# Optimization experiments

Hardware: AMD Instinct MI355X
Metric: run time of the kernel (lower is better)

Reference implementation:

```python
import jax, jax.numpy as jnp
import numpy as np


def _maxpool2x2(x):
    # x: [N, C, H, W] -> [N, C, H//2, W//2]
    return jax.lax.reduce_window(x, -jnp.inf, jax.lax.max,
                                 (1, 1, 2, 2), (1, 1, 2, 2), 'VALID')


def _head(a, W1, b1, W2, b2, W3, b3):
    # headModel: maxpool -> (adaptive avgpool to 7x7 is identity here) -> flatten -> classifier (eval mode)
    mp = _maxpool2x2(a)                      # [N, 512, 7, 7]
    flat = mp.reshape(mp.shape[0], -1)       # [N, 25088]
    h = jax.nn.relu(flat @ W1.T + b1)        # [N, 4096]
    h = jax.nn.relu(h @ W2.T + b2)           # [N, 4096]
    return h @ W3.T + b3                     # [N, 1000]


def setup_inputs() -> dict:
    key = jax.random.key(0)
    ks = jax.random.split(key, 7)
    C, HW, FC, NC = 512, 14, 4096, 1000
    acts = jax.random.uniform(ks[0], (1, C, HW, HW), dtype=jnp.float32)  # post-ReLU feature map
    s1 = 1.0 / np.sqrt(C * 7 * 7)
    s2 = 1.0 / np.sqrt(FC)
    return {
        'activations': acts,
        'W1': jax.random.normal(ks[1], (FC, C * 7 * 7), dtype=jnp.float32) * s1,
        'b1': jax.random.normal(ks[2], (FC,), dtype=jnp.float32) * 0.01,
        'W2': jax.random.normal(ks[3], (FC, FC), dtype=jnp.float32) * s2,
        'b2': jax.random.normal(ks[4], (FC,), dtype=jnp.float32) * 0.01,
        'W3': jax.random.normal(ks[5], (NC, FC), dtype=jnp.float32) * s2,
        'b3': jax.random.normal(ks[6], (NC,), dtype=jnp.float32) * 0.01,
        'ht': 224,
        'wt': 224,
    }


def reference(activations, W1, b1, W2, b2, W3, b3, ht, wt):
    C = activations.shape[1]
    logits = _head(activations, W1, b1, W2, b2, W3, b3)   # [1, 1000]
    img_class = jnp.argmax(logits[0])
    base = logits[0, img_class]

    # Batch all C channel ablations: abl[i] = activations with channel i zeroed.
    mask = (1.0 - jnp.eye(C, dtype=activations.dtype))[:, :, None, None]  # [C, C, 1, 1]
    abl = activations * mask                                              # [C, C, 14, 14]
    logits_new = _head(abl, W1, b1, W2, b2, W3, b3)                        # [C, 1000]
    alpha = (base - jnp.take(logits_new, img_class, axis=1)) / base        # [C]

    # fused = relu(sum_i alpha_i * bilinear_resize(act_i)); resize is linear,
    # so weight in activation space and do one resize (same math as the loop).
    weighted = jnp.einsum('c,chw->hw', alpha, activations[0])              # [14, 14]
    sal = jax.image.resize(weighted[None, None], (1, 1, ht, wt),
                           method='bilinear')[0, 0]                        # [ht, wt]
    fused = jax.nn.relu(sal)
    mn, mx = fused.min(), fused.max()
    denom = jnp.where(mx != mn, mx - mn, 1.0)
    fused = jnp.where(mx != mn, (fused - mn) / denom, fused)
    return fused, img_class
```

## Files before the change

kernel.cpp:

```cpp
#include <hip/hip_runtime.h>
#include <math.h>

#define CCH 512
#define F1 25088
#define FC 4096
#define NCLS 1000
#define OW 224
#define KSPLIT 4
#define KSLICE 1024
#define PSTRIDE (CCH*FC)

#define WS_DT 0
#define WS_MP (WS_DT + FC*CCH)
#define WS_QS (WS_MP + F1)
#define WS_H1PRE (WS_QS + FC*4)
#define WS_H1 (WS_H1PRE + FC)
#define WS_H2 (WS_H1 + FC)
#define WS_LOGITS (WS_H2 + FC)
#define WS_CLSBASE (WS_LOGITS + NCLS)
#define WS_ALPHA (WS_CLSBASE + 2)
#define WS_MINMAX (WS_ALPHA + CCH)
#define WS_WEIGHTED (WS_MINMAX + 2)
#define WS_LOGPART (WS_WEIGHTED + 196)
#define WS_A (WS_LOGPART + 64*CCH)
#define WS_PART (WS_A + CCH*FC/2)
#define WS_END (WS_PART + KSPLIT*CCH*FC)
#define WS_NEED_BYTES ((size_t)WS_END * 4)

typedef __attribute__((ext_vector_type(8))) short bfrag;
typedef __attribute__((ext_vector_type(4))) float f32x4;

static __device__ __forceinline__ unsigned short f2bf(float x) {
    unsigned u = __float_as_uint(x);
    unsigned r = 0x7FFFu + ((u >> 16) & 1u);
    return (unsigned short)((u + r) >> 16);
}

#define GLD16(g, l) __builtin_amdgcn_global_load_lds( \
    (const __attribute__((address_space(1))) void*)(g), \
    (__attribute__((address_space(3))) void*)(l), 16, 0, 0)

__global__ void k_maxpool(const float* __restrict__ act, float* __restrict__ ws) {
    int t = threadIdx.x;
    if (blockIdx.x == 0) {
        if (t == 0) ((int*)(ws + WS_MINMAX))[0] = 0x7F800000;
        if (t == 1) ((int*)(ws + WS_MINMAX))[1] = 0;
    }
    int idx = blockIdx.x * 256 + t;
    if (idx >= CCH * 49) return;
    int c = idx / 49, r = idx % 49, y = r / 7, x = r % 7;
    const float* a = act + c * 196 + (2 * y) * 14 + 2 * x;
    float m = fmaxf(fmaxf(a[0], a[1]), fmaxf(a[14], a[15]));
    ws[WS_MP + idx] = m;
}

__global__ __launch_bounds__(256) void k_phi3(const float* __restrict__ W1,
                                              const float* __restrict__ mp,
                                              float* __restrict__ Dt,
                                              float* __restrict__ qs) {
    __shared__ float buf[6272];
    __shared__ float red[128];
    int b = blockIdx.x;
    int j = b >> 2, q = b & 3;
    int t = threadIdx.x;
    const float4* src = (const float4*)(W1 + (size_t)j * F1 + q * 6272);
    const float4* msc = (const float4*)(mp + q * 6272);
    for (int n = t; n < 1568; n += 256) {
        float4 w = src[n], m = msc[n];
        float4 p;
        p.x = w.x * m.x; p.y = w.y * m.y; p.z = w.z * m.z; p.w = w.w * m.w;
        *(float4*)&buf[n * 4] = p;
    }
    __syncthreads();
    if (t < 128) {
        const float* bb = buf + t * 49;
        float s = 0.f;
        #pragma unroll
        for (int k = 0; k < 49; ++k) s += bb[k];
        Dt[(size_t)j * CCH + q * 128 + t] = s;
        red[t] = s;
    }
    __syncthreads();
    if (t < 64) {
        float v = red[t] + red[t + 64];
        for (int off = 32; off > 0; off >>= 1) v += __shfl_down(v, off, 64);
        if (t == 0) qs[b] = v;
    }
}

__global__ void k_h1b(const float* __restrict__ qs, const float* __restrict__ b1,
                      float* __restrict__ h1pre, float* __restrict__ h1) {
    int j = blockIdx.x * 256 + threadIdx.x;
    if (j < FC) {
        const float* g = qs + j * 4;
        float v = b1[j] + ((g[0] + g[1]) + (g[2] + g[3]));
        h1pre[j] = v; h1[j] = fmaxf(v, 0.f);
    }
}

template <bool RELU>
__global__ void k_gemv4096(const float* __restrict__ M, const float* __restrict__ v,
                           const float* __restrict__ bias, float* __restrict__ out) {
    int j = blockIdx.x, t = threadIdx.x;
    const float4* row = (const float4*)(M + (size_t)j * FC);
    const float4* vv = (const float4*)v;
    float s = 0.f;
    #pragma unroll
    for (int q = 0; q < 4; ++q) {
        int n = q * 256 + t;
        float4 w = row[n], x = vv[n];
        s += w.x * x.x + w.y * x.y + w.z * x.z + w.w * x.w;
    }
    __shared__ float red[256];
    red[t] = s; __syncthreads();
    if (t < 128) red[t] += red[t + 128]; __syncthreads();
    if (t < 64)  red[t] += red[t + 64];  __syncthreads();
    if (t < 64) {
        float x = red[t];
        for (int off = 32; off > 0; off >>= 1) x += __shfl_down(x, off, 64);
        if (t == 0) { float r = bias[j] + x; out[j] = RELU ? fmaxf(r, 0.f) : r; }
    }
}

__global__ void k_argmax(const float* __restrict__ logits, float* __restrict__ clsbase,
                         float* __restrict__ dout_cls) {
    int t = threadIdx.x;
    float best = -INFINITY; int bi = NCLS;
    for (int n = t; n < NCLS; n += 256) {
        float v = logits[n];
        if (v > best || (v == best && n < bi)) { best = v; bi = n; }
    }
    __shared__ float bv[256]; __shared__ int bidx[256];
    bv[t] = best; bidx[t] = bi; __syncthreads();
    for (int o = 128; o > 0; o >>= 1) {
        if (t < o) {
            float v2 = bv[t + o]; int i2 = bidx[t + o];
            if (v2 > bv[t] || (v2 == bv[t] && i2 < bidx[t])) { bv[t] = v2; bidx[t] = i2; }
        }
        __syncthreads();
    }
    if (t == 0) { clsbase[0] = (float)bidx[0]; clsbase[1] = bv[0]; *dout_cls = (float)bidx[0]; }
}

__global__ __launch_bounds__(256) void k_abuild(const float* __restrict__ Dt,
                                                const float* __restrict__ h1pre,
                                                unsigned short* __restrict__ A) {
    __shared__ unsigned short tile[64][72];
    int kt = blockIdx.x, it = blockIdx.y, t = threadIdx.x;
    int k0 = kt * 64, i0 = it * 64;
    #pragma unroll
    for (int q = 0; q < 16; ++q) {
        int kk = q * 4 + (t >> 6);
        int ii = t & 63;
        float v = fmaxf(h1pre[k0 + kk] - Dt[(size_t)(k0 + kk) * CCH + i0 + ii], 0.f);
        tile[kk][ii] = f2bf(v);
    }
    __syncthreads();
    #pragma unroll
    for (int q = 0; q < 4; ++q) {
        int c = q * 256 + t;
        int ii = c >> 4, kc = c & 15;
        ushort4 v;
        v.x = tile[kc * 4 + 0][ii]; v.y = tile[kc * 4 + 1][ii];
        v.z = tile[kc * 4 + 2][ii]; v.w = tile[kc * 4 + 3][ii];
        *(ushort4*)&A[(size_t)(i0 + ii) * FC + k0 + kc * 4] = v;
    }
}

__global__ __launch_bounds__(512) void k_mfma_all(
    const unsigned short* __restrict__ A, const float* __restrict__ W2,
    float* __restrict__ part) {
    __shared__ char As[65536];
    __shared__ char Bs[8192];
    int nj = blockIdx.x;
    int ks = blockIdx.y;
    int t = threadIdx.x;
    int wid = t >> 6, lane = t & 63, lr = lane & 15, lh = lane >> 4;
    int j0 = nj * 64;

    int wrow = t >> 3, wch = t & 7;
    const float* wsrc = W2 + (size_t)(j0 + wrow) * FC + (size_t)ks * KSLICE + wch * 8;
    char* bdst = Bs + ((size_t)wrow * 8 + (wch ^ (wrow & 7))) * 16;

    f32x4 acc[4][4];
    #pragma unroll
    for (int f = 0; f < 4; ++f)
        #pragma unroll
        for (int n = 0; n < 4; ++n) acc[f][n] = (f32x4){0.f, 0.f, 0.f, 0.f};

    for (int kst = 0; kst < KSLICE; kst += 64) {
        size_t k0 = (size_t)ks * KSLICE + kst;
        __syncthreads();
        #pragma unroll
        for (int r = 0; r < 8; ++r) {
            int c = t + 512 * r;
            int row = c >> 3, ch = c & 7;
            size_t g = (size_t)row * FC + k0 + (size_t)((ch ^ (row & 7)) * 8);
            GLD16(A + g, As + (size_t)c * 16);
        }
        {
            const float4 wa = ((const float4*)(wsrc + kst))[0];
            const float4 wb = ((const float4*)(wsrc + kst))[1];
            union { bfrag v; unsigned short u[8]; } pk;
            pk.u[0] = f2bf(wa.x); pk.u[1] = f2bf(wa.y);
            pk.u[2] = f2bf(wa.z); pk.u[3] = f2bf(wa.w);
            pk.u[4] = f2bf(wb.x); pk.u[5] = f2bf(wb.y);
            pk.u[6] = f2bf(wb.z); pk.u[7] = f2bf(wb.w);
            *(bfrag*)bdst = pk.v;
        }
        __syncthreads();
        #pragma unroll
        for (int kf = 0; kf < 2; ++kf) {
            bfrag bfr[4];
            #pragma unroll
            for (int n = 0; n < 4; ++n) {
                int brow = n * 16 + lr;
                bfr[n] = *(const bfrag*)(Bs + ((size_t)brow * 8 + ((kf * 4 + lh) ^ (brow & 7))) * 16);
            }
            #pragma unroll
            for (int f = 0; f < 4; ++f) {
                int arow = wid * 64 + f * 16 + lr;
                bfrag af = *(const bfrag*)(As + ((size_t)arow * 8 + ((kf * 4 + lh) ^ (arow & 7))) * 16);
                #pragma unroll
                for (int n = 0; n < 4; ++n)
                    acc[f][n] = __builtin_amdgcn_mfma_f32_16x16x32_bf16(af, bfr[n], acc[f][n], 0, 0, 0);
            }
        }
    }
    float* base = part + (size_t)ks * PSTRIDE;
    #pragma unroll
    for (int f = 0; f < 4; ++f) {
        #pragma unroll
        for (int n = 0; n < 4; ++n) {
            #pragma unroll
            for (int r = 0; r < 4; ++r) {
                int row = wid * 64 + f * 16 + lh * 4 + r;
                base[(size_t)row * FC + j0 + n * 16 + lr] = acc[f][n][r];
            }
        }
    }
}

__global__ __launch_bounds__(256) void k_alpha(
    const float* __restrict__ part, const float* __restrict__ b2,
    const float* __restrict__ W3, const float* __restrict__ b3,
    const float* __restrict__ clsbase, float* __restrict__ alpha) {
    int i = blockIdx.x, t = threadIdx.x;
    int cls = (int)clsbase[0]; float base = clsbase[1];
    const float* w3r = W3 + (size_t)cls * FC;
    const float* p0 = part + (size_t)i * FC;
    float s = 0.f;
    for (int j = t; j < FC; j += 256) {
        float v = ((p0[j] + p0[j + PSTRIDE]) + (p0[j + 2 * PSTRIDE] + p0[j + 3 * PSTRIDE]))
                  + b2[j];
        s += fmaxf(v, 0.f) * w3r[j];
    }
    __shared__ float red[256];
    red[t] = s; __syncthreads();
    if (t < 128) red[t] += red[t + 128]; __syncthreads();
    if (t < 64)  red[t] += red[t + 64];  __syncthreads();
    if (t < 64) {
        float x = red[t];
        for (int off = 32; off > 0; off >>= 1) x += __shfl_down(x, off, 64);
        if (t == 0) {
            float logit = x + b3[cls];
            alpha[i] = (base - logit) / base;
        }
    }
}

__global__ void k_weighted2(const float* __restrict__ alpha, const float* __restrict__ act,
                            float* __restrict__ weighted) {
    __shared__ float sA[CCH];
    int t = threadIdx.x;
    for (int i = t; i < CCH; i += 256) sA[i] = alpha[i];
    __syncthreads();
    for (int p = t; p < 196; p += 256) {
        float s = 0.f;
        for (int i = 0; i < CCH; ++i) s = fmaf(sA[i], act[i * 196 + p], s);
        weighted[p] = s;
    }
}

__global__ __launch_bounds__(256) void k_gemm_abl(
    const float* __restrict__ Dt, const float* __restrict__ h1pre,
    const float* __restrict__ W2, const float* __restrict__ b2,
    const float* __restrict__ W3, const float* __restrict__ clsbase,
    float* __restrict__ logit_part) {
    int mi = blockIdx.x, nj = blockIdx.y, t = threadIdx.x;
    int tx = t & 15, ty = t >> 4;
    int i0 = mi * 64, j0 = nj * 64;
    __shared__ float As2[16][64];
    __shared__ float Bs2[16][65];
    float acc[4][4] = {};
    for (int k0 = 0; k0 < FC; k0 += 16) {
        #pragma unroll
        for (int r = 0; r < 4; ++r) {
            int e = t + 256 * r; int kk = e >> 6, ii = e & 63;
            As2[kk][ii] = fmaxf(h1pre[k0 + kk] - Dt[(size_t)(k0 + kk) * CCH + i0 + ii], 0.f);
        }
        {
            int jj = t >> 2, kks = (t & 3) * 4;
            const float4 wv = *(const float4*)(W2 + (size_t)(j0 + jj) * FC + k0 + kks);
            Bs2[kks + 0][jj] = wv.x; Bs2[kks + 1][jj] = wv.y;
            Bs2[kks + 2][jj] = wv.z; Bs2[kks + 3][jj] = wv.w;
        }
        __syncthreads();
        #pragma unroll
        for (int kk = 0; kk < 16; ++kk) {
            float4 a4 = *(const float4*)&As2[kk][tx * 4];
            float av[4] = {a4.x, a4.y, a4.z, a4.w};
            float bv[4] = {Bs2[kk][ty * 4 + 0], Bs2[kk][ty * 4 + 1],
                           Bs2[kk][ty * 4 + 2], Bs2[kk][ty * 4 + 3]};
            #pragma unroll
            for (int a = 0; a < 4; ++a)
                #pragma unroll
                for (int b = 0; b < 4; ++b)
                    acc[a][b] = fmaf(av[a], bv[b], acc[a][b]);
        }
        __syncthreads();
    }
    int cls = (int)clsbase[0];
    const float* w3r = W3 + (size_t)cls * FC;
    float prt[4] = {0.f, 0.f, 0.f, 0.f};
    #pragma unroll
    for (int b = 0; b < 4; ++b) {
        int j2 = j0 + ty * 4 + b;
        float bb = b2[j2], w3 = w3r[j2];
        #pragma unroll
        for (int a = 0; a < 4; ++a) prt[a] = fmaf(fmaxf(acc[a][b] + bb, 0.f), w3, prt[a]);
    }
    __shared__ float red2[16][68];
    #pragma unroll
    for (int a = 0; a < 4; ++a) red2[ty][tx * 4 + a] = prt[a];
    __syncthreads();
    if (t < 64) {
        float s = 0.f;
        #pragma unroll
        for (int q = 0; q < 16; ++q) s += red2[q][t];
        logit_part[nj * CCH + i0 + t] = s;
    }
}

__global__ void k_alpha_fb(const float* __restrict__ logit_part, const float* __restrict__ b3,
                           const float* __restrict__ clsbase, float* __restrict__ alpha) {
    int t = blockIdx.x * 256 + threadIdx.x;
    if (t >= CCH) return;
    int cls = (int)clsbase[0]; float base = clsbase[1];
    float s = 0.f;
    for (int q = 0; q < 64; ++q) s += logit_part[q * CCH + t];
    alpha[t] = (base - (s + b3[cls])) / base;
}

__global__ void k_resize(const float* __restrict__ weighted, float* __restrict__ out,
                         int* __restrict__ minmax) {
    __shared__ float sW[196];
    int t = threadIdx.x;
    if (t < 196) sW[t] = weighted[t];
    __syncthreads();
    int pix = blockIdx.x * 256 + t;
    int y = pix / OW, x = pix % OW;
    float uy = (y + 0.5f) * 0.0625f - 0.5f;
    float ux = (x + 0.5f) * 0.0625f - 0.5f;
    float y0f = floorf(uy), x0f = floorf(ux);
    float fy = uy - y0f, fx = ux - x0f;
    int y0 = (int)y0f, x0 = (int)x0f;
    int y0c = min(max(y0, 0), 13), y1c = min(max(y0 + 1, 0), 13);
    int x0c = min(max(x0, 0), 13), x1c = min(max(x0 + 1, 0), 13);
    float v00 = sW[y0c * 14 + x0c], v01 = sW[y0c * 14 + x1c];
    float v10 = sW[y1c * 14 + x0c], v11 = sW[y1c * 14 + x1c];
    float v0 = v00 + (v01 - v00) * fx;
    float v1 = v10 + (v11 - v10) * fx;
    float v = v0 + (v1 - v0) * fy;
    float f = fmaxf(v, 0.f);
    out[pix] = f;
    __shared__ float rmn[256], rmx[256];
    rmn[t] = f; rmx[t] = f; __syncthreads();
    for (int o = 128; o > 0; o >>= 1) {
        if (t < o) { rmn[t] = fminf(rmn[t], rmn[t + o]); rmx[t] = fmaxf(rmx[t], rmx[t + o]); }
        __syncthreads();
    }
    if (t == 0) {
        atomicMin(&minmax[0], __float_as_int(rmn[0]));
        atomicMax(&minmax[1], __float_as_int(rmx[0]));
    }
}

__global__ void k_norm(float* __restrict__ out, const int* __restrict__ minmax) {
    float mn = __int_as_float(minmax[0]);
    float mx = __int_as_float(minmax[1]);
    int pix = blockIdx.x * 256 + threadIdx.x;
    if (mx != mn) out[pix] = (out[pix] - mn) / (mx - mn);
}

extern "C" void kernel_launch(void* const* d_in, const int* in_sizes, int n_in,
                              void* d_out, int out_size, void* d_ws, size_t ws_size,
                              hipStream_t stream) {
    const float* act = (const float*)d_in[0];
    const float* W1  = (const float*)d_in[1];
    const float* b1  = (const float*)d_in[2];
    const float* W2  = (const float*)d_in[3];
    const float* b2  = (const float*)d_in[4];
    const float* W3  = (const float*)d_in[5];
    const float* b3  = (const float*)d_in[6];
    float* out = (float*)d_out;
    float* ws = (float*)d_ws;
    const bool fast = (ws_size >= WS_NEED_BYTES);

    k_maxpool<<<98, 256, 0, stream>>>(act, ws);
    k_phi3<<<16384, 256, 0, stream>>>(W1, ws + WS_MP, ws + WS_DT, ws + WS_QS);
    k_h1b<<<16, 256, 0, stream>>>(ws + WS_QS, b1, ws + WS_H1PRE, ws + WS_H1);
    k_gemv4096<true><<<4096, 256, 0, stream>>>(W2, ws + WS_H1, b2, ws + WS_H2);
    k_gemv4096<false><<<1000, 256, 0, stream>>>(W3, ws + WS_H2, b3, ws + WS_LOGITS);
    k_argmax<<<1, 256, 0, stream>>>(ws + WS_LOGITS, ws + WS_CLSBASE, out + 50176);
    if (fast) {
        k_abuild<<<dim3(64, 8), 256, 0, stream>>>(ws + WS_DT, ws + WS_H1PRE,
                                                  (unsigned short*)(ws + WS_A));
        k_mfma_all<<<dim3(64, KSPLIT), 512, 0, stream>>>(
            (const unsigned short*)(ws + WS_A), W2, ws + WS_PART);
        k_alpha<<<CCH, 256, 0, stream>>>(ws + WS_PART, b2, W3, b3,
                                         ws + WS_CLSBASE, ws + WS_ALPHA);
    } else {
        k_gemm_abl<<<dim3(8, 64), 256, 0, stream>>>(ws + WS_DT, ws + WS_H1PRE, W2, b2, W3,
                                                    ws + WS_CLSBASE, ws + WS_LOGPART);
        k_alpha_fb<<<2, 256, 0, stream>>>(ws + WS_LOGPART, b3, ws + WS_CLSBASE,
                                          ws + WS_ALPHA);
    }
    k_weighted2<<<1, 256, 0, stream>>>(ws + WS_ALPHA, act, ws + WS_WEIGHTED);
    k_resize<<<196, 256, 0, stream>>>(ws + WS_WEIGHTED, out, (int*)(ws + WS_MINMAX));
    k_norm<<<196, 256, 0, stream>>>(out, (const int*)(ws + WS_MINMAX));
}
```

Measured before the change: 219.1 us.

## Fuse unablated layer-2 GEMV into batched MFMA kernel and split W1 reduction finer

The baseline layer-2 GEMV (h1·W2) now runs inside the batched ablation MFMA kernel, reusing the W2 tile each block already loads, so W2 (64 MB fp32) is no longer read twice from HBM. Partial h2 sums per K-slice go to a small buffer and a new kernel adds them with the bias and ReLU. The MFMA kernel's N-tile shrinks from 64 to 32 columns, which doubles the grid. The W1 phi kernel is split into 8 chunks of 128 threads instead of 4 chunks of 256, and the h1 reduction sums 8 partials. In exchange, the A operand is reloaded twice as often per output column, and the argmax and logits now wait for the big GEMM to finish.

```diff
diff --git a/kernel.cpp b/kernel.cpp
--- a/kernel.cpp
+++ b/kernel.cpp
@@ -8,15 +8,17 @@
 #define OW 224
 #define KSPLIT 4
 #define KSLICE 1024
+#define TJ 32
 #define PSTRIDE (CCH*FC)
 
 #define WS_DT 0
 #define WS_MP (WS_DT + FC*CCH)
 #define WS_QS (WS_MP + F1)
-#define WS_H1PRE (WS_QS + FC*4)
+#define WS_H1PRE (WS_QS + FC*8)
 #define WS_H1 (WS_H1PRE + FC)
 #define WS_H2 (WS_H1 + FC)
-#define WS_LOGITS (WS_H2 + FC)
+#define WS_H2PART (WS_H2 + FC)
+#define WS_LOGITS (WS_H2PART + 4*FC)
 #define WS_CLSBASE (WS_LOGITS + NCLS)
 #define WS_ALPHA (WS_CLSBASE + 2)
 #define WS_MINMAX (WS_ALPHA + CCH)
@@ -54,35 +56,30 @@
     ws[WS_MP + idx] = m;
 }
 
-__global__ __launch_bounds__(256) void k_phi3(const float* __restrict__ W1,
+__global__ __launch_bounds__(128) void k_phi4(const float* __restrict__ W1,
                                               const float* __restrict__ mp,
                                               float* __restrict__ Dt,
                                               float* __restrict__ qs) {
-    __shared__ float buf[6272];
-    __shared__ float red[128];
+    __shared__ float buf[3136];
     int b = blockIdx.x;
-    int j = b >> 2, q = b & 3;
-    int t = threadIdx.x;
-    const float4* src = (const float4*)(W1 + (size_t)j * F1 + q * 6272);
-    const float4* msc = (const float4*)(mp + q * 6272);
-    for (int n = t; n < 1568; n += 256) {
+    int j = b >> 3, e = b & 7;
+    int t = threadIdx.x;
+    const float4* src = (const float4*)(W1 + (size_t)j * F1 + e * 3136);
+    const float4* msc = (const float4*)(mp + e * 3136);
+    for (int n = t; n < 784; n += 128) {
         float4 w = src[n], m = msc[n];
         float4 p;
         p.x = w.x * m.x; p.y = w.y * m.y; p.z = w.z * m.z; p.w = w.w * m.w;
         *(float4*)&buf[n * 4] = p;
     }
     __syncthreads();
-    if (t < 128) {
+    if (t < 64) {
         const float* bb = buf + t * 49;
         float s = 0.f;
         #pragma unroll
         for (int k = 0; k < 49; ++k) s += bb[k];
-        Dt[(size_t)j * CCH + q * 128 + t] = s;
-        red[t] = s;
-    }
-    __syncthreads();
-    if (t < 64) {
-        float v = red[t] + red[t + 64];
+        Dt[(size_t)j * CCH + e * 64 + t] = s;
+        float v = s;
         for (int off = 32; off > 0; off >>= 1) v += __shfl_down(v, off, 64);
         if (t == 0) qs[b] = v;
     }
@@ -92,8 +89,8 @@
                       float* __restrict__ h1pre, float* __restrict__ h1) {
     int j = blockIdx.x * 256 + threadIdx.x;
     if (j < FC) {
-        const float* g = qs + j * 4;
-        float v = b1[j] + ((g[0] + g[1]) + (g[2] + g[3]));
+        const float* g = qs + j * 8;
+        float v = b1[j] + (((g[0] + g[1]) + (g[2] + g[3])) + ((g[4] + g[5]) + (g[6] + g[7])));
         h1pre[j] = v; h1[j] = fmaxf(v, 0.f);
     }
 }
@@ -167,26 +164,35 @@
     }
 }
 
-__global__ __launch_bounds__(512) void k_mfma_all(
+__global__ __launch_bounds__(512) void k_mfma_all2(
     const unsigned short* __restrict__ A, const float* __restrict__ W2,
-    float* __restrict__ part) {
+    const float* __restrict__ h1, float* __restrict__ part,
+    float* __restrict__ h2part) {
     __shared__ char As[65536];
-    __shared__ char Bs[8192];
+    __shared__ char Bs[4096];
+    __shared__ float h1s[KSLICE];
     int nj = blockIdx.x;
     int ks = blockIdx.y;
     int t = threadIdx.x;
     int wid = t >> 6, lane = t & 63, lr = lane & 15, lh = lane >> 4;
-    int j0 = nj * 64;
-
-    int wrow = t >> 3, wch = t & 7;
-    const float* wsrc = W2 + (size_t)(j0 + wrow) * FC + (size_t)ks * KSLICE + wch * 8;
-    char* bdst = Bs + ((size_t)wrow * 8 + (wch ^ (wrow & 7))) * 16;
-
-    f32x4 acc[4][4];
+    int j0 = nj * TJ;
+
+    {
+        float2 v = *(const float2*)(h1 + ks * KSLICE + t * 2);
+        *(float2*)&h1s[t * 2] = v;
+    }
+
+    int wr = t >> 4;
+    int wc = t & 15;
+    const float* wsrc = W2 + (size_t)(j0 + wr) * FC + (size_t)ks * KSLICE + wc * 4;
+    char* bdst = Bs + ((size_t)wr * 8 + ((wc >> 1) ^ (wr & 7))) * 16 + (wc & 1) * 8;
+    float hacc = 0.f;
+
+    f32x4 acc[4][2];
     #pragma unroll
     for (int f = 0; f < 4; ++f)
         #pragma unroll
-        for (int n = 0; n < 4; ++n) acc[f][n] = (f32x4){0.f, 0.f, 0.f, 0.f};
+        for (int n = 0; n < 2; ++n) acc[f][n] = (f32x4){0.f, 0.f, 0.f, 0.f};
 
     for (int kst = 0; kst < KSLICE; kst += 64) {
         size_t k0 = (size_t)ks * KSLICE + kst;
@@ -199,21 +205,19 @@
             GLD16(A + g, As + (size_t)c * 16);
         }
         {
-            const float4 wa = ((const float4*)(wsrc + kst))[0];
-            const float4 wb = ((const float4*)(wsrc + kst))[1];
-            union { bfrag v; unsigned short u[8]; } pk;
-            pk.u[0] = f2bf(wa.x); pk.u[1] = f2bf(wa.y);
-            pk.u[2] = f2bf(wa.z); pk.u[3] = f2bf(wa.w);
-            pk.u[4] = f2bf(wb.x); pk.u[5] = f2bf(wb.y);
-            pk.u[6] = f2bf(wb.z); pk.u[7] = f2bf(wb.w);
-            *(bfrag*)bdst = pk.v;
+            float4 w = *(const float4*)(wsrc + kst);
+            hacc += w.x * h1s[kst + wc * 4] + w.y * h1s[kst + wc * 4 + 1]
+                  + w.z * h1s[kst + wc * 4 + 2] + w.w * h1s[kst + wc * 4 + 3];
+            ushort4 pk;
+            pk.x = f2bf(w.x); pk.y = f2bf(w.y); pk.z = f2bf(w.z); pk.w = f2bf(w.w);
+            *(ushort4*)bdst = pk;
         }
         __syncthreads();
         #pragma unroll
         for (int kf = 0; kf < 2; ++kf) {
-            bfrag bfr[4];
+            bfrag bfr[2];
             #pragma unroll
-            for (int n = 0; n < 4; ++n) {
+            for (int n = 0; n < 2; ++n) {
                 int brow = n * 16 + lr;
                 bfr[n] = *(const bfrag*)(Bs + ((size_t)brow * 8 + ((kf * 4 + lh) ^ (brow & 7))) * 16);
             }
@@ -222,22 +226,33 @@
                 int arow = wid * 64 + f * 16 + lr;
                 bfrag af = *(const bfrag*)(As + ((size_t)arow * 8 + ((kf * 4 + lh) ^ (arow & 7))) * 16);
                 #pragma unroll
-                for (int n = 0; n < 4; ++n)
+                for (int n = 0; n < 2; ++n)
                     acc[f][n] = __builtin_amdgcn_mfma_f32_16x16x32_bf16(af, bfr[n], acc[f][n], 0, 0, 0);
             }
         }
     }
+
+    for (int off = 8; off > 0; off >>= 1) hacc += __shfl_down(hacc, off, 64);
+    if (wc == 0) h2part[ks * FC + j0 + wr] = hacc;
+
     float* base = part + (size_t)ks * PSTRIDE;
     #pragma unroll
-    for (int f = 0; f < 4; ++f) {
-        #pragma unroll
-        for (int n = 0; n < 4; ++n) {
+    for (int f = 0; f < 4; ++f)
+        #pragma unroll
+        for (int n = 0; n < 2; ++n)
             #pragma unroll
             for (int r = 0; r < 4; ++r) {
                 int row = wid * 64 + f * 16 + lh * 4 + r;
                 base[(size_t)row * FC + j0 + n * 16 + lr] = acc[f][n][r];
             }
-        }
+}
+
+__global__ void k_h2sum(const float* __restrict__ h2part, const float* __restrict__ b2,
+                        float* __restrict__ h2) {
+    int j = blockIdx.x * 256 + threadIdx.x;
+    if (j < FC) {
+        float v = b2[j] + ((h2part[j] + h2part[FC + j]) + (h2part[2 * FC + j] + h2part[3 * FC + j]));
+        h2[j] = fmaxf(v, 0.f);
     }
 }
 
@@ -408,19 +423,23 @@
     const bool fast = (ws_size >= WS_NEED_BYTES);
 
     k_maxpool<<<98, 256, 0, stream>>>(act, ws);
-    k_phi3<<<16384, 256, 0, stream>>>(W1, ws + WS_MP, ws + WS_DT, ws + WS_QS);
+    k_phi4<<<32768, 128, 0, stream>>>(W1, ws + WS_MP, ws + WS_DT, ws + WS_QS);
     k_h1b<<<16, 256, 0, stream>>>(ws + WS_QS, b1, ws + WS_H1PRE, ws + WS_H1);
-    k_gemv4096<true><<<4096, 256, 0, stream>>>(W2, ws + WS_H1, b2, ws + WS_H2);
-    k_gemv4096<false><<<1000, 256, 0, stream>>>(W3, ws + WS_H2, b3, ws + WS_LOGITS);
-    k_argmax<<<1, 256, 0, stream>>>(ws + WS_LOGITS, ws + WS_CLSBASE, out + 50176);
     if (fast) {
         k_abuild<<<dim3(64, 8), 256, 0, stream>>>(ws + WS_DT, ws + WS_H1PRE,
                                                   (unsigned short*)(ws + WS_A));
-        k_mfma_all<<<dim3(64, KSPLIT), 512, 0, stream>>>(
-            (const unsigned short*)(ws + WS_A), W2, ws + WS_PART);
+        k_mfma_all2<<<dim3(128, KSPLIT), 512, 0, stream>>>(
+            (const unsigned short*)(ws + WS_A), W2, ws + WS_H1,
+            ws + WS_PART, ws + WS_H2PART);
+        k_h2sum<<<16, 256, 0, stream>>>(ws + WS_H2PART, b2, ws + WS_H2);
+        k_gemv4096<false><<<1000, 256, 0, stream>>>(W3, ws + WS_H2, b3, ws + WS_LOGITS);
+        k_argmax<<<1, 256, 0, stream>>>(ws + WS_LOGITS, ws + WS_CLSBASE, out + 50176);
         k_alpha<<<CCH, 256, 0, stream>>>(ws + WS_PART, b2, W3, b3,
                                          ws + WS_CLSBASE, ws + WS_ALPHA);
     } else {
+        k_gemv4096<true><<<4096, 256, 0, stream>>>(W2, ws + WS_H1, b2, ws + WS_H2);
+        k_gemv4096<false><<<1000, 256, 0, stream>>>(W3, ws + WS_H2, b3, ws + WS_LOGITS);
+        k_argmax<<<1, 256, 0, stream>>>(ws + WS_LOGITS, ws + WS_CLSBASE, out + 50176);
         k_gemm_abl<<<dim3(8, 64), 256, 0, stream>>>(ws + WS_DT, ws + WS_H1PRE, W2, b2, W3,
                                                     ws + WS_CLSBASE, ws + WS_LOGPART);
         k_alpha_fb<<<2, 256, 0, stream>>>(ws + WS_LOGPART, b3, ws + WS_CLSBASE,
```

New measurement: 221.1 us. No clear change (+0.9%).

## Fuse base h2 GEMV into ablation MFMA GEMM, retile, store bf16 partials

Applied to the files above, without the earlier changes.

Merges k_phi3 and k_h1b into one block-per-row kernel that produces h1 directly. Folds the unablated W2·h1 GEMV into the ablation MFMA GEMM, so the blocks with mi==0 reuse the W2 loads they already make, and this removes a separate 64MB W2 read. Retiles the MFMA kernel to 128x128 tiles over a 32x4x4 grid with 256 threads and stores split-K partials as bf16 to halve the partial write and read traffic. Fuses the channel-weighted sum into the resize kernel. The costs are a recompute of the weighted sum in every resize block, lower precision in the partial sums, and W2 now being read once per M tile.

```diff
diff --git a/kernel.cpp b/kernel.cpp
--- a/kernel.cpp
+++ b/kernel.cpp
@@ -12,19 +12,18 @@
 
 #define WS_DT 0
 #define WS_MP (WS_DT + FC*CCH)
-#define WS_QS (WS_MP + F1)
-#define WS_H1PRE (WS_QS + FC*4)
+#define WS_H1PRE (WS_MP + F1)
 #define WS_H1 (WS_H1PRE + FC)
 #define WS_H2 (WS_H1 + FC)
-#define WS_LOGITS (WS_H2 + FC)
+#define WS_H2PART (WS_H2 + FC)
+#define WS_LOGITS (WS_H2PART + 4*FC)
 #define WS_CLSBASE (WS_LOGITS + NCLS)
 #define WS_ALPHA (WS_CLSBASE + 2)
 #define WS_MINMAX (WS_ALPHA + CCH)
-#define WS_WEIGHTED (WS_MINMAX + 2)
-#define WS_LOGPART (WS_WEIGHTED + 196)
+#define WS_LOGPART (WS_MINMAX + 2)
 #define WS_A (WS_LOGPART + 64*CCH)
-#define WS_PART (WS_A + CCH*FC/2)
-#define WS_END (WS_PART + KSPLIT*CCH*FC)
+#define WS_PARTB (WS_A + CCH*FC/2)
+#define WS_END (WS_PARTB + KSPLIT*CCH*FC/2)
 #define WS_NEED_BYTES ((size_t)WS_END * 4)
 
 typedef __attribute__((ext_vector_type(8))) short bfrag;
@@ -54,47 +53,44 @@
     ws[WS_MP + idx] = m;
 }
 
-__global__ __launch_bounds__(256) void k_phi3(const float* __restrict__ W1,
+__global__ __launch_bounds__(256) void k_phi5(const float* __restrict__ W1,
                                               const float* __restrict__ mp,
+                                              const float* __restrict__ b1,
                                               float* __restrict__ Dt,
-                                              float* __restrict__ qs) {
-    __shared__ float buf[6272];
-    __shared__ float red[128];
-    int b = blockIdx.x;
-    int j = b >> 2, q = b & 3;
-    int t = threadIdx.x;
-    const float4* src = (const float4*)(W1 + (size_t)j * F1 + q * 6272);
-    const float4* msc = (const float4*)(mp + q * 6272);
-    for (int n = t; n < 1568; n += 256) {
-        float4 w = src[n], m = msc[n];
-        float4 p;
-        p.x = w.x * m.x; p.y = w.y * m.y; p.z = w.z * m.z; p.w = w.w * m.w;
-        *(float4*)&buf[n * 4] = p;
-    }
-    __syncthreads();
-    if (t < 128) {
+                                              float* __restrict__ h1pre,
+                                              float* __restrict__ h1) {
+    __shared__ float buf[12544];
+    __shared__ float red[256];
+    int j = blockIdx.x, t = threadIdx.x;
+    const float* row = W1 + (size_t)j * F1;
+    float sh[2];
+    #pragma unroll
+    for (int h = 0; h < 2; ++h) {
+        __syncthreads();
+        const float4* src = (const float4*)(row + h * 12544);
+        const float4* msc = (const float4*)(mp + h * 12544);
+        for (int n = t; n < 3136; n += 256) {
+            float4 w = src[n], m = msc[n];
+            float4 p;
+            p.x = w.x * m.x; p.y = w.y * m.y; p.z = w.z * m.z; p.w = w.w * m.w;
+            *(float4*)&buf[n * 4] = p;
+        }
+        __syncthreads();
         const float* bb = buf + t * 49;
         float s = 0.f;
         #pragma unroll
         for (int k = 0; k < 49; ++k) s += bb[k];
-        Dt[(size_t)j * CCH + q * 128 + t] = s;
-        red[t] = s;
-    }
+        Dt[(size_t)j * CCH + h * 256 + t] = s;
+        sh[h] = s;
+    }
+    red[t] = sh[0] + sh[1];
+    __syncthreads();
+    if (t < 128) red[t] += red[t + 128];
     __syncthreads();
     if (t < 64) {
         float v = red[t] + red[t + 64];
         for (int off = 32; off > 0; off >>= 1) v += __shfl_down(v, off, 64);
-        if (t == 0) qs[b] = v;
-    }
-}
-
-__global__ void k_h1b(const float* __restrict__ qs, const float* __restrict__ b1,
-                      float* __restrict__ h1pre, float* __restrict__ h1) {
-    int j = blockIdx.x * 256 + threadIdx.x;
-    if (j < FC) {
-        const float* g = qs + j * 4;
-        float v = b1[j] + ((g[0] + g[1]) + (g[2] + g[3]));
-        h1pre[j] = v; h1[j] = fmaxf(v, 0.f);
+        if (t == 0) { float hv = b1[j] + v; h1pre[j] = hv; h1[j] = fmaxf(hv, 0.f); }
     }
 }
 
@@ -167,21 +163,29 @@
     }
 }
 
-__global__ __launch_bounds__(512) void k_mfma_all(
+__global__ __launch_bounds__(256) void k_mfma_v4(
     const unsigned short* __restrict__ A, const float* __restrict__ W2,
-    float* __restrict__ part) {
-    __shared__ char As[65536];
-    __shared__ char Bs[8192];
+    const float* __restrict__ h1, unsigned short* __restrict__ partb,
+    float* __restrict__ h2part) {
+    __shared__ char As[16384];
+    __shared__ char Bs[16384];
+    __shared__ float h1s[KSLICE];
     int nj = blockIdx.x;
-    int ks = blockIdx.y;
+    int mi = blockIdx.y;
+    int ks = blockIdx.z;
     int t = threadIdx.x;
     int wid = t >> 6, lane = t & 63, lr = lane & 15, lh = lane >> 4;
-    int j0 = nj * 64;
-
-    int wrow = t >> 3, wch = t & 7;
-    const float* wsrc = W2 + (size_t)(j0 + wrow) * FC + (size_t)ks * KSLICE + wch * 8;
-    char* bdst = Bs + ((size_t)wrow * 8 + (wch ^ (wrow & 7))) * 16;
-
+    int i0 = mi * 128, j0 = nj * 128;
+    int wr = (wid >> 1) * 64;
+    int wc = (wid & 1) * 64;
+
+    {
+        float4 v = *(const float4*)(h1 + ks * KSLICE + t * 4);
+        *(float4*)&h1s[t * 4] = v;
+    }
+
+    bool doh = (mi == 0);
+    float hacc[4] = {0.f, 0.f, 0.f, 0.f};
     f32x4 acc[4][4];
     #pragma unroll
     for (int f = 0; f < 4; ++f)
@@ -189,71 +193,115 @@
         for (int n = 0; n < 4; ++n) acc[f][n] = (f32x4){0.f, 0.f, 0.f, 0.f};
 
     for (int kst = 0; kst < KSLICE; kst += 64) {
-        size_t k0 = (size_t)ks * KSLICE + kst;
-        __syncthreads();
-        #pragma unroll
-        for (int r = 0; r < 8; ++r) {
-            int c = t + 512 * r;
+        int k0 = ks * KSLICE + kst;
+        __syncthreads();
+        #pragma unroll
+        for (int r = 0; r < 4; ++r) {
+            int c = t + 256 * r;
             int row = c >> 3, ch = c & 7;
-            size_t g = (size_t)row * FC + k0 + (size_t)((ch ^ (row & 7)) * 8);
-            GLD16(A + g, As + (size_t)c * 16);
-        }
-        {
-            const float4 wa = ((const float4*)(wsrc + kst))[0];
-            const float4 wb = ((const float4*)(wsrc + kst))[1];
+            GLD16(A + (size_t)(i0 + row) * FC + k0 + ((ch ^ (row & 7)) * 8),
+                  As + (size_t)c * 16);
+        }
+        #pragma unroll
+        for (int r = 0; r < 4; ++r) {
+            int c = t + 256 * r;
+            int row = c >> 3, ch = c & 7;
+            int ko = (ch ^ (row & 7)) * 8;
+            const float* wp = W2 + (size_t)(j0 + row) * FC + k0 + ko;
+            float4 wa = *(const float4*)wp;
+            float4 wb = *(const float4*)(wp + 4);
+            if (doh) {
+                hacc[r] += wa.x * h1s[kst + ko + 0] + wa.y * h1s[kst + ko + 1]
+                         + wa.z * h1s[kst + ko + 2] + wa.w * h1s[kst + ko + 3]
+                         + wb.x * h1s[kst + ko + 4] + wb.y * h1s[kst + ko + 5]
+                         + wb.z * h1s[kst + ko + 6] + wb.w * h1s[kst + ko + 7];
+            }
             union { bfrag v; unsigned short u[8]; } pk;
             pk.u[0] = f2bf(wa.x); pk.u[1] = f2bf(wa.y);
             pk.u[2] = f2bf(wa.z); pk.u[3] = f2bf(wa.w);
             pk.u[4] = f2bf(wb.x); pk.u[5] = f2bf(wb.y);
             pk.u[6] = f2bf(wb.z); pk.u[7] = f2bf(wb.w);
-            *(bfrag*)bdst = pk.v;
+            *(bfrag*)(Bs + (size_t)c * 16) = pk.v;
         }
         __syncthreads();
         #pragma unroll
         for (int kf = 0; kf < 2; ++kf) {
-            bfrag bfr[4];
+            bfrag bv[4];
             #pragma unroll
             for (int n = 0; n < 4; ++n) {
-                int brow = n * 16 + lr;
-                bfr[n] = *(const bfrag*)(Bs + ((size_t)brow * 8 + ((kf * 4 + lh) ^ (brow & 7))) * 16);
+                int br = wc + n * 16 + lr;
+                bv[n] = *(const bfrag*)(Bs + ((size_t)br * 8 + ((kf * 4 + lh) ^ (br & 7))) * 16);
             }
             #pragma unroll
             for (int f = 0; f < 4; ++f) {
-                int arow = wid * 64 + f * 16 + lr;
-                bfrag af = *(const bfrag*)(As + ((size_t)arow * 8 + ((kf * 4 + lh) ^ (arow & 7))) * 16);
+                int ar = wr + f * 16 + lr;
+                bfrag av = *(const bfrag*)(As + ((size_t)ar * 8 + ((kf * 4 + lh) ^ (ar & 7))) * 16);
                 #pragma unroll
                 for (int n = 0; n < 4; ++n)
-                    acc[f][n] = __builtin_amdgcn_mfma_f32_16x16x32_bf16(af, bfr[n], acc[f][n], 0, 0, 0);
+                    acc[f][n] = __builtin_amdgcn_mfma_f32_16x16x32_bf16(av, bv[n], acc[f][n], 0, 0, 0);
             }
         }
     }
-    float* base = part + (size_t)ks * PSTRIDE;
+
+    if (doh) {
+        #pragma unroll
+        for (int r = 0; r < 4; ++r) {
+            float v = hacc[r];
+            v += __shfl_down(v, 4, 8);
+            v += __shfl_down(v, 2, 8);
+            v += __shfl_down(v, 1, 8);
+            if ((t & 7) == 0) h2part[ks * FC + j0 + r * 32 + (t >> 3)] = v;
+        }
+    }
+    unsigned short* pb = partb + (size_t)ks * PSTRIDE;
     #pragma unroll
     for (int f = 0; f < 4; ++f) {
-        #pragma unroll
-        for (int n = 0; n < 4; ++n) {
+        int row0 = i0 + wr + f * 16 + lh * 4;
+        #pragma unroll
+        for (int rr = 0; rr < 4; ++rr) {
             #pragma unroll
-            for (int r = 0; r < 4; ++r) {
-                int row = wid * 64 + f * 16 + lh * 4 + r;
-                base[(size_t)row * FC + j0 + n * 16 + lr] = acc[f][n][r];
-            }
-        }
-    }
-}
-
-__global__ __launch_bounds__(256) void k_alpha(
-    const float* __restrict__ part, const float* __restrict__ b2,
+            for (int n = 0; n < 4; ++n)
+                pb[(size_t)(row0 + rr) * FC + j0 + wc + n * 16 + lr] = f2bf(acc[f][n][rr]);
+        }
+    }
+}
+
+__global__ void k_h2sum(const float* __restrict__ h2part, const float* __restrict__ b2,
+                        float* __restrict__ h2) {
+    int j = blockIdx.x * 256 + threadIdx.x;
+    if (j < FC) {
+        float v = b2[j] + ((h2part[j] + h2part[FC + j]) + (h2part[2 * FC + j] + h2part[3 * FC + j]));
+        h2[j] = fmaxf(v, 0.f);
+    }
+}
+
+__global__ __launch_bounds__(256) void k_alpha_b(
+    const unsigned short* __restrict__ partb, const float* __restrict__ b2,
     const float* __restrict__ W3, const float* __restrict__ b3,
     const float* __restrict__ clsbase, float* __restrict__ alpha) {
     int i = blockIdx.x, t = threadIdx.x;
     int cls = (int)clsbase[0]; float base = clsbase[1];
     const float* w3r = W3 + (size_t)cls * FC;
-    const float* p0 = part + (size_t)i * FC;
     float s = 0.f;
-    for (int j = t; j < FC; j += 256) {
-        float v = ((p0[j] + p0[j + PSTRIDE]) + (p0[j + 2 * PSTRIDE] + p0[j + 3 * PSTRIDE]))
-                  + b2[j];
-        s += fmaxf(v, 0.f) * w3r[j];
+    #pragma unroll
+    for (int q = 0; q < 2; ++q) {
+        int j = (q * 256 + t) * 8;
+        uint4 p0 = *(const uint4*)(partb + (size_t)i * FC + j);
+        uint4 p1 = *(const uint4*)(partb + (size_t)PSTRIDE + (size_t)i * FC + j);
+        uint4 p2 = *(const uint4*)(partb + 2 * (size_t)PSTRIDE + (size_t)i * FC + j);
+        uint4 p3 = *(const uint4*)(partb + 3 * (size_t)PSTRIDE + (size_t)i * FC + j);
+        #pragma unroll
+        for (int e = 0; e < 4; ++e) {
+            unsigned a0 = ((const unsigned*)&p0)[e], a1 = ((const unsigned*)&p1)[e];
+            unsigned a2 = ((const unsigned*)&p2)[e], a3 = ((const unsigned*)&p3)[e];
+            float lo = (__uint_as_float(a0 << 16) + __uint_as_float(a1 << 16))
+                     + (__uint_as_float(a2 << 16) + __uint_as_float(a3 << 16));
+            float hi = (__uint_as_float(a0 & 0xFFFF0000u) + __uint_as_float(a1 & 0xFFFF0000u))
+                     + (__uint_as_float(a2 & 0xFFFF0000u) + __uint_as_float(a3 & 0xFFFF0000u));
+            int jj = j + e * 2;
+            s += fmaxf(lo + b2[jj], 0.f) * w3r[jj];
+            s += fmaxf(hi + b2[jj + 1], 0.f) * w3r[jj + 1];
+        }
     }
     __shared__ float red[256];
     red[t] = s; __syncthreads();
@@ -262,23 +310,7 @@
     if (t < 64) {
         float x = red[t];
         for (int off = 32; off > 0; off >>= 1) x += __shfl_down(x, off, 64);
-        if (t == 0) {
-            float logit = x + b3[cls];
-            alpha[i] = (base - logit) / base;
-        }
-    }
-}
-
-__global__ void k_weighted2(const float* __restrict__ alpha, const float* __restrict__ act,
-                            float* __restrict__ weighted) {
-    __shared__ float sA[CCH];
-    int t = threadIdx.x;
-    for (int i = t; i < CCH; i += 256) sA[i] = alpha[i];
-    __syncthreads();
-    for (int p = t; p < 196; p += 256) {
-        float s = 0.f;
-        for (int i = 0; i < CCH; ++i) s = fmaf(sA[i], act[i * 196 + p], s);
-        weighted[p] = s;
+        if (t == 0) alpha[i] = (base - (x + b3[cls])) / base;
     }
 }
 
@@ -352,11 +384,18 @@
     alpha[t] = (base - (s + b3[cls])) / base;
 }
 
-__global__ void k_resize(const float* __restrict__ weighted, float* __restrict__ out,
-                         int* __restrict__ minmax) {
+__global__ void k_resize2(const float* __restrict__ alpha, const float* __restrict__ act,
+                          float* __restrict__ out, int* __restrict__ minmax) {
+    __shared__ float sA[CCH];
     __shared__ float sW[196];
     int t = threadIdx.x;
-    if (t < 196) sW[t] = weighted[t];
+    for (int i = t; i < CCH; i += 256) sA[i] = alpha[i];
+    __syncthreads();
+    if (t < 196) {
+        float s = 0.f;
+        for (int c = 0; c < CCH; ++c) s = fmaf(sA[c], act[c * 196 + t], s);
+        sW[t] = s;
+    }
     __syncthreads();
     int pix = blockIdx.x * 256 + t;
     int y = pix / OW, x = pix % OW;
@@ -408,25 +447,28 @@
     const bool fast = (ws_size >= WS_NEED_BYTES);
 
     k_maxpool<<<98, 256, 0, stream>>>(act, ws);
-    k_phi3<<<16384, 256, 0, stream>>>(W1, ws + WS_MP, ws + WS_DT, ws + WS_QS);
-    k_h1b<<<16, 256, 0, stream>>>(ws + WS_QS, b1, ws + WS_H1PRE, ws + WS_H1);
-    k_gemv4096<true><<<4096, 256, 0, stream>>>(W2, ws + WS_H1, b2, ws + WS_H2);
-    k_gemv4096<false><<<1000, 256, 0, stream>>>(W3, ws + WS_H2, b3, ws + WS_LOGITS);
-    k_argmax<<<1, 256, 0, stream>>>(ws + WS_LOGITS, ws + WS_CLSBASE, out + 50176);
+    k_phi5<<<4096, 256, 0, stream>>>(W1, ws + WS_MP, b1, ws + WS_DT,
+                                     ws + WS_H1PRE, ws + WS_H1);
     if (fast) {
         k_abuild<<<dim3(64, 8), 256, 0, stream>>>(ws + WS_DT, ws + WS_H1PRE,
                                                   (unsigned short*)(ws + WS_A));
-        k_mfma_all<<<dim3(64, KSPLIT), 512, 0, stream>>>(
-            (const unsigned short*)(ws + WS_A), W2, ws + WS_PART);
-        k_alpha<<<CCH, 256, 0, stream>>>(ws + WS_PART, b2, W3, b3,
-                                         ws + WS_CLSBASE, ws + WS_ALPHA);
+        k_mfma_v4<<<dim3(32, 4, 4), 256, 0, stream>>>(
+            (const unsigned short*)(ws + WS_A), W2, ws + WS_H1,
+            (unsigned short*)(ws + WS_PARTB), ws + WS_H2PART);
+        k_h2sum<<<16, 256, 0, stream>>>(ws + WS_H2PART, b2, ws + WS_H2);
+        k_gemv4096<false><<<1000, 256, 0, stream>>>(W3, ws + WS_H2, b3, ws + WS_LOGITS);
+        k_argmax<<<1, 256, 0, stream>>>(ws + WS_LOGITS, ws + WS_CLSBASE, out + 50176);
+        k_alpha_b<<<CCH, 256, 0, stream>>>((const unsigned short*)(ws + WS_PARTB), b2,
+                                           W3, b3, ws + WS_CLSBASE, ws + WS_ALPHA);
     } else {
+        k_gemv4096<true><<<4096, 256, 0, stream>>>(W2, ws + WS_H1, b2, ws + WS_H2);
+        k_gemv4096<false><<<1000, 256, 0, stream>>>(W3, ws + WS_H2, b3, ws + WS_LOGITS);
+        k_argmax<<<1, 256, 0, stream>>>(ws + WS_LOGITS, ws + WS_CLSBASE, out + 50176);
         k_gemm_abl<<<dim3(8, 64), 256, 0, stream>>>(ws + WS_DT, ws + WS_H1PRE, W2, b2, W3,
                                                     ws + WS_CLSBASE, ws + WS_LOGPART);
         k_alpha_fb<<<2, 256, 0, stream>>>(ws + WS_LOGPART, b3, ws + WS_CLSBASE,
                                           ws + WS_ALPHA);
     }
-    k_weighted2<<<1, 256, 0, stream>>>(ws + WS_ALPHA, act, ws + WS_WEIGHTED);
-    k_resize<<<196, 256, 0, stream>>>(ws + WS_WEIGHTED, out, (int*)(ws + WS_MINMAX));
+    k_resize2<<<196, 256, 0, stream>>>(ws + WS_ALPHA, act, out, (int*)(ws + WS_MINMAX));
     k_norm<<<196, 256, 0, stream>>>(out, (const int*)(ws + WS_MINMAX));
 }
```

Measured after the change: 224.3 us. 1.02x slower.
